# Kernel optimization log

Hardware: AMD Instinct MI355X
Metric: run time of the kernel (lower is better)

## Reference

```python
import jax, jax.numpy as jnp
import numpy as np

N, D_IN, D_OUT, NHEAD = 4096, 512, 128, 4


def setup_inputs() -> dict:
    key = jax.random.key(0)
    k1, k2, k3, k4, k5 = jax.random.split(key, 5)
    adj = jax.random.randint(k1, (N, N), 0, 2).astype(jnp.float32)  # dense binary adjacency
    x = jax.random.normal(k2, (N, D_IN), dtype=jnp.float32)
    W = jax.random.normal(k3, (D_IN, D_OUT), dtype=jnp.float32) * (1.0 / np.sqrt(D_IN))
    attn_l_w = jax.random.normal(k4, (NHEAD, D_OUT), dtype=jnp.float32) * (1.0 / np.sqrt(D_OUT))
    attn_r_w = jax.random.normal(k5, (NHEAD, D_OUT), dtype=jnp.float32) * (1.0 / np.sqrt(D_OUT))
    b = jnp.zeros((D_OUT,), dtype=jnp.float32)
    return {"adj": adj, "x": x, "W": W, "attn_l_w": attn_l_w, "attn_r_w": attn_r_w, "b": b}


def reference(adj, x, W, attn_l_w, attn_r_w, b):
    # h = x @ W : [N, D_OUT]
    h = x @ W
    el = h @ attn_l_w.T  # [N, H]  (nn.Linear(output_dim, nhead, bias=False))
    er = h @ attn_r_w.T  # [N, H]
    # Dense equivalent of nonzero-gather + index_put_ scatter into [N, N, H]:
    # attn[i, j, :] = exp(leaky_relu(el[i] + er[j])) where adj[i, j] != 0, else 0.
    e = el[:, None, :] + er[None, :, :]                      # [N, N, H]
    a = jnp.where(adj[:, :, None] != 0,
                  jnp.exp(jax.nn.leaky_relu(e, negative_slope=0.2)),
                  jnp.zeros((), dtype=e.dtype))              # [N, N, H]
    a = jnp.transpose(a, (0, 2, 1))                          # [N, H, N]
    # F.normalize(p=1, dim=-1): divide by max(L1 row sum, 1e-12); a >= 0 so L1 = sum.
    a = a / jnp.maximum(jnp.sum(a, axis=-1, keepdims=True), 1e-12)
    out = jnp.einsum('nhm,md->nhd', a, h) + b                # [N, H, D_OUT]
    return out.reshape(out.shape[0], -1)                     # flatten heads -> [N, H*D_OUT]
```

## Files before the change

kernel.cpp:

```cpp
#include <hip/hip_runtime.h>

#define NN 4096
#define DIN 512
#define DOUT 128
#define NH 4
#define LOG2E 1.44269504088896340736f

typedef __bf16 bf16x8 __attribute__((ext_vector_type(8)));
typedef float f32x4 __attribute__((ext_vector_type(4)));
typedef unsigned short u16;
typedef u16 u16x8 __attribute__((ext_vector_type(8)));
typedef u16 u16x4 __attribute__((ext_vector_type(4)));
typedef unsigned long long u64;

static __device__ __forceinline__ u16 f2bf(float f) {
  __bf16 h = (__bf16)f;
  return __builtin_bit_cast(u16, h);
}

static __device__ __forceinline__ void gl_lds16(const void* g, void* l) {
  __builtin_amdgcn_global_load_lds(
      (const __attribute__((address_space(1))) unsigned int*)g,
      (__attribute__((address_space(3))) unsigned int*)l, 16, 0, 0);
}

__global__ __launch_bounds__(256) void pack_adj(const float* __restrict__ adj,
                                                u64* __restrict__ adjW) {
  const int t = threadIdx.x;
  const int lane = t & 63;
  const int wv = t >> 6;
  const size_t blk = blockIdx.x;
  #pragma unroll
  for (int it = 0; it < 4; ++it) {
    const size_t wbase = blk * 128 + it * 32 + wv * 8;
    float v[8];
    #pragma unroll
    for (int u = 0; u < 8; ++u) v[u] = adj[(wbase + u) * 64 + lane];
    #pragma unroll
    for (int u = 0; u < 8; ++u) {
      const u64 m = __ballot(v[u] != 0.0f);
      if (lane == 0) adjW[wbase + u] = m;
    }
  }
}

__global__ __launch_bounds__(256) void prep_wt(const float* __restrict__ W,
                                               u16* __restrict__ wthi,
                                               u16* __restrict__ wtlo) {
  const int n = blockIdx.x;
  const int t = threadIdx.x;
  for (int k = t; k < 512; k += 256) {
    const float w = W[(size_t)k * 128 + n];
    const __bf16 hi = (__bf16)w;
    const float lo = w - (float)hi;
    wthi[(size_t)n * 512 + k] = __builtin_bit_cast(u16, hi);
    wtlo[(size_t)n * 512 + k] = f2bf(lo);
  }
}

__global__ __launch_bounds__(512, 1) void hcompute(
    const float* __restrict__ x, const u16* __restrict__ wthi,
    const u16* __restrict__ wtlo, const float* __restrict__ alw,
    const float* __restrict__ arw, u16* __restrict__ hT,
    float* __restrict__ el, float* __restrict__ erT) {
  __shared__ __align__(16) char pool[147456];
  const int t = threadIdx.x;
  const int i0 = blockIdx.x * 16;
  const int lane = t & 63, w = t >> 6;
  const int l15 = lane & 15, lhi = lane >> 4;

  const int xr = t >> 5, xk = (t & 31) * 4;
  const unsigned x_off =
      ((unsigned)(xr * 256 + xk * 2)) ^ ((unsigned)((xr & 7) << 4));

  f32x4 acc = (f32x4){0.f, 0.f, 0.f, 0.f};

  auto stageW = [&](int kc, int buf) {
    #pragma unroll
    for (int q = 0; q < 4; ++q) {
      const int off = q * 8192 + t * 16;
      const int n = off >> 8;
      const int kb = off & 255;
      const int ksrc = (kb ^ ((n & 7) << 4)) >> 1;
      const size_t so = (size_t)n * 512 + kc * 128 + ksrc;
      gl_lds16(wthi + so, pool + 16384 + buf * 32768 + off);
      gl_lds16(wtlo + so, pool + 81920 + buf * 32768 + off);
    }
  };
  auto writeX = [&](const float4& xv, int buf) {
    u16x4 hi, lo;
    const float* xp = (const float*)&xv;
    #pragma unroll
    for (int j = 0; j < 4; ++j) {
      const __bf16 hb = (__bf16)xp[j];
      hi[j] = __builtin_bit_cast(u16, hb);
      lo[j] = f2bf(xp[j] - (float)hb);
    }
    *(u16x4*)(pool + buf * 4096 + x_off) = hi;
    *(u16x4*)(pool + 8192 + buf * 4096 + x_off) = lo;
  };

  stageW(0, 0);
  {
    float4 xv = *(const float4*)(x + (size_t)(i0 + xr) * DIN + xk);
    writeX(xv, 0);
  }
  float4 xnext;
  for (int kc = 0; kc < 4; ++kc) {
    const int cur = kc & 1;
    __syncthreads();
    const bool more = (kc < 3);
    if (more) {
      stageW(kc + 1, cur ^ 1);
      xnext = *(const float4*)(x + (size_t)(i0 + xr) * DIN + (kc + 1) * 128 + xk);
    }
    #pragma unroll
    for (int ks = 0; ks < 4; ++ks) {
      const unsigned kbyte = (unsigned)(ks * 64 + lhi * 16);
      const unsigned xoff =
          (unsigned)(l15 * 256) + (kbyte ^ (unsigned)((l15 & 7) << 4));
      const bf16x8 ah = *(const bf16x8*)(pool + cur * 4096 + xoff);
      const bf16x8 al = *(const bf16x8*)(pool + 8192 + cur * 4096 + xoff);
      const int n = w * 16 + l15;
      const unsigned wb =
          (unsigned)(n * 256) + (kbyte ^ (unsigned)((n & 7) << 4));
      const bf16x8 bh = *(const bf16x8*)(pool + 16384 + cur * 32768 + wb);
      const bf16x8 bl = *(const bf16x8*)(pool + 81920 + cur * 32768 + wb);
      acc = __builtin_amdgcn_mfma_f32_16x16x32_bf16(ah, bh, acc, 0, 0, 0);
      acc = __builtin_amdgcn_mfma_f32_16x16x32_bf16(al, bh, acc, 0, 0, 0);
      acc = __builtin_amdgcn_mfma_f32_16x16x32_bf16(ah, bl, acc, 0, 0, 0);
    }
    if (more) writeX(xnext, cur ^ 1);
  }
  __syncthreads();
  float* h_lds = (float*)(pool + 16384);
  #pragma unroll
  for (int reg = 0; reg < 4; ++reg)
    h_lds[(lhi * 4 + reg) * 132 + w * 16 + l15] = acc[reg];
  __syncthreads();
  {
    const int d = t >> 2, ih0 = (t & 3) * 4;
    u16x4 hv;
    #pragma unroll
    for (int j = 0; j < 4; ++j) hv[j] = f2bf(h_lds[(ih0 + j) * 132 + d]);
    *(u16x4*)(hT + (size_t)d * NN + i0 + ih0) = hv;
  }
  if (t < 128) {
    const int r = t >> 3, hh = (t >> 1) & 3, side = t & 1;
    const float* wrow = (side ? arw : alw) + hh * DOUT;
    float s = 0.f;
    for (int d = 0; d < 128; ++d) s += h_lds[r * 132 + d] * wrow[d];
    s *= LOG2E;
    if (side == 0) el[(size_t)(i0 + r) * NH + hh] = s;
    else erT[(size_t)hh * NN + i0 + r] = s;
  }
}

template <int KSPLIT>
__global__ __launch_bounds__(512, 4) void gat_main(
    const unsigned char* __restrict__ adjB, const u16* __restrict__ hT,
    const float* __restrict__ el, const float* __restrict__ erT,
    const float* __restrict__ bias, float* __restrict__ outp,
    float* __restrict__ accP, float* __restrict__ SP) {
  __shared__ __align__(16) u16 A_lds[2][64 * 64];
  __shared__ __align__(16) u16 B_lds[2][128 * 64];
  __shared__ float S_lds[64];
  const int t = threadIdx.x;
  const int b = blockIdx.x;
  const int g = b & 255;
  const int ks = (KSPLIT > 1) ? (b >> 8) : 0;
  const int i0 = g * 16;
  const int jbeg = (ks * 64) / KSPLIT;
  const int jcnt = ((ks + 1) * 64) / KSPLIT - jbeg;
  const int row = t >> 3, head = row >> 4, il = row & 15;
  const float elv = el[(size_t)(i0 + il) * NH + head];
  const unsigned char* adjrow = adjB + (size_t)(i0 + il) * 512 + jbeg * 8 + (t & 7);
  const float* errow = erT + (size_t)head * NN + jbeg * 64 + (t & 7) * 8;
  const unsigned a_off =
      (unsigned)(row * 128 + (t & 7) * 16) ^ (unsigned)((row & 7) << 4);
  const int bd = t >> 3;
  const int bkb = (t & 7) * 16;
  const u16* hsrc = hT + (size_t)bd * NN + jbeg * 64 +
                    (((unsigned)bkb ^ (unsigned)((bd & 7) << 4)) >> 1);
  const int lane = t & 63, w = t >> 6;
  const int rt = w >> 1, ch = w & 1;
  const int l15 = lane & 15, lhi = lane >> 4;
  const int am = rt * 16 + l15;
  const unsigned aswz = (unsigned)((am & 7) << 4);
  f32x4 acc[4];
  #pragma unroll
  for (int ct = 0; ct < 4; ++ct) acc[ct] = (f32x4){0.f, 0.f, 0.f, 0.f};
  float Sp = 0.f;

  auto stageB = [&](int jt, int buf) {
    char* dst = (char*)B_lds[buf] + t * 16;
    gl_lds16(hsrc + jt * 64, dst);
    gl_lds16(hsrc + jt * 64 + (size_t)64 * NN, dst + 8192);
  };
  auto genA = [&](unsigned char abv, const float4& ea, const float4& eb, int buf) {
    float ev[8];
    *(float4*)ev = ea;
    *(float4*)(ev + 4) = eb;
    u16x8 pk;
    float s = 0.f;
    #pragma unroll
    for (int q = 0; q < 8; ++q) {
      const float e = elv + ev[q];
      const float l = fmaf(0.4f, __builtin_fabsf(e), 0.6f * e);
      const float ex = exp2f(l);
      const int msk = ((int)((unsigned)abv << (31 - q))) >> 31;
      const float av = __builtin_bit_cast(float, __builtin_bit_cast(int, ex) & msk);
      s += av;
      pk[q] = f2bf(av);
    }
    Sp += s;
    *(u16x8*)((char*)A_lds[buf] + a_off) = pk;
  };

  stageB(0, 0);
  {
    const unsigned char ab = adjrow[0];
    const float4 e0 = *(const float4*)errow;
    const float4 e1 = *(const float4*)(errow + 4);
    genA(ab, e0, e1, 0);
  }

  for (int jt = 0; jt < jcnt; ++jt) {
    const int cur = jt & 1;
    __syncthreads();
    const bool more = (jt + 1 < jcnt);
    unsigned char abn = 0;
    float4 e0n = {0, 0, 0, 0}, e1n = {0, 0, 0, 0};
    if (more) {
      stageB(jt + 1, cur ^ 1);
      abn = adjrow[(jt + 1) * 8];
      e0n = *(const float4*)(errow + (jt + 1) * 64);
      e1n = *(const float4*)(errow + (jt + 1) * 64 + 4);
    }
    const char* Abc = (const char*)A_lds[cur];
    const char* Bbc = (const char*)B_lds[cur];
    #pragma unroll
    for (int kk = 0; kk < 2; ++kk) {
      const unsigned kbyte = (unsigned)(kk * 64 + lhi * 16);
      const bf16x8 af = *(const bf16x8*)(Abc + (am * 128 + (kbyte ^ aswz)));
      #pragma unroll
      for (int ct = 0; ct < 4; ++ct) {
        const int col = ch * 64 + ct * 16 + l15;
        const bf16x8 bfr = *(const bf16x8*)(
            Bbc + (col * 128 + (kbyte ^ (unsigned)((col & 7) << 4))));
        acc[ct] = __builtin_amdgcn_mfma_f32_16x16x32_bf16(af, bfr, acc[ct], 0, 0, 0);
      }
    }
    if (more) genA(abn, e0n, e1n, cur ^ 1);
  }

  Sp += __shfl_xor(Sp, 1);
  Sp += __shfl_xor(Sp, 2);
  Sp += __shfl_xor(Sp, 4);

  if (KSPLIT == 1) {
    if ((t & 7) == 0) S_lds[row] = Sp;
    __syncthreads();
    #pragma unroll
    for (int reg = 0; reg < 4; ++reg) {
      const int mrow = rt * 16 + lhi * 4 + reg;
      const float inv = 1.f / fmaxf(S_lds[mrow], 1e-12f);
      const int irow = i0 + (mrow & 15);
      #pragma unroll
      for (int ct = 0; ct < 4; ++ct) {
        const int colp = ch * 64 + ct * 16 + l15;
        outp[(size_t)irow * (NH * DOUT) + rt * DOUT + colp] =
            acc[ct][reg] * inv + bias[colp];
      }
    }
  } else {
    if ((t & 7) == 0) SP[(size_t)b * 64 + row] = Sp;
    float* dst = accP + (size_t)b * 8192;
    #pragma unroll
    for (int reg = 0; reg < 4; ++reg) {
      const int mrow = rt * 16 + lhi * 4 + reg;
      #pragma unroll
      for (int ct = 0; ct < 4; ++ct) {
        const int colp = ch * 64 + ct * 16 + l15;
        dst[mrow * 128 + colp] = acc[ct][reg];
      }
    }
  }
}

template <int KS>
__global__ __launch_bounds__(256) void reduce_norm(
    const float* __restrict__ accP, const float* __restrict__ SP,
    const float* __restrict__ bias, float* __restrict__ outp) {
  const int idx = blockIdx.x * 256 + threadIdx.x;
  const int o = idx * 4;
  const int d = o & 127;
  const int hh = (o >> 7) & 3;
  const int i = o >> 9;
  const int g = i >> 4;
  const int m = hh * 16 + (i & 15);
  float4 p = make_float4(0.f, 0.f, 0.f, 0.f);
  float S = 0.f;
  #pragma unroll
  for (int s = 0; s < KS; ++s) {
    const float4 q =
        *(const float4*)(accP + (size_t)(s * 256 + g) * 8192 + m * 128 + d);
    p.x += q.x; p.y += q.y; p.z += q.z; p.w += q.w;
    S += SP[(size_t)(s * 256 + g) * 64 + m];
  }
  const float inv = 1.f / fmaxf(S, 1e-12f);
  const float4 bb = *(const float4*)(bias + d);
  float4 r;
  r.x = p.x * inv + bb.x;
  r.y = p.y * inv + bb.y;
  r.z = p.z * inv + bb.z;
  r.w = p.w * inv + bb.w;
  *(float4*)(outp + o) = r;
}

extern "C" void kernel_launch(void* const* d_in, const int* in_sizes, int n_in,
                              void* d_out, int out_size, void* d_ws, size_t ws_size,
                              hipStream_t stream) {
  const float* adj = (const float*)d_in[0];
  const float* x = (const float*)d_in[1];
  const float* W = (const float*)d_in[2];
  const float* alw = (const float*)d_in[3];
  const float* arw = (const float*)d_in[4];
  const float* bias = (const float*)d_in[5];
  float* out = (float*)d_out;
  char* ws = (char*)d_ws;
  u16* hT = (u16*)ws;
  float* el = (float*)(ws + 0x100000);
  float* erT = (float*)(ws + 0x110000);
  unsigned char* adjB = (unsigned char*)(ws + 0x120000);
  u16* wthi = (u16*)(ws + 0x320000);
  u16* wtlo = (u16*)(ws + 0x340000);
  float* accP = (float*)(ws + 0x360000);
  const size_t need3 = 0x360000ull + 768ull * 32768 + 768ull * 256;
  const size_t need2 = 0x360000ull + 512ull * 32768 + 512ull * 256;

  pack_adj<<<2048, 256, 0, stream>>>(adj, (u64*)adjB);
  prep_wt<<<128, 256, 0, stream>>>(W, wthi, wtlo);
  hcompute<<<256, 512, 0, stream>>>(x, wthi, wtlo, alw, arw, hT, el, erT);
  if (ws_size >= need3) {
    float* SP = (float*)(ws + 0x360000 + 768ull * 32768);
    gat_main<3><<<768, 512, 0, stream>>>(adjB, hT, el, erT, bias, out, accP, SP);
    reduce_norm<3><<<2048, 256, 0, stream>>>(accP, SP, bias, out);
  } else if (ws_size >= need2) {
    float* SP = (float*)(ws + 0x360000 + 512ull * 32768);
    gat_main<2><<<512, 512, 0, stream>>>(adjB, hT, el, erT, bias, out, accP, SP);
    reduce_norm<2><<<2048, 256, 0, stream>>>(accP, SP, bias, out);
  } else {
    gat_main<1><<<256, 512, 0, stream>>>(adjB, hT, el, erT, bias, out, accP, accP);
  }
}
```

Measured before the change: 170.3 us.

## Rewrite attention kernel with register-resident A, 32x32 MFMA and in-block K-split

```diff
diff --git a/kernel.cpp b/kernel.cpp
--- a/kernel.cpp
+++ b/kernel.cpp
@@ -8,10 +8,11 @@
 
 typedef __bf16 bf16x8 __attribute__((ext_vector_type(8)));
 typedef float f32x4 __attribute__((ext_vector_type(4)));
+typedef float f32x16 __attribute__((ext_vector_type(16)));
 typedef unsigned short u16;
+typedef unsigned int u32;
 typedef u16 u16x8 __attribute__((ext_vector_type(8)));
 typedef u16 u16x4 __attribute__((ext_vector_type(4)));
-typedef unsigned long long u64;
 
 static __device__ __forceinline__ u16 f2bf(float f) {
   __bf16 h = (__bf16)f;
@@ -24,37 +25,34 @@
       (__attribute__((address_space(3))) unsigned int*)l, 16, 0, 0);
 }
 
-__global__ __launch_bounds__(256) void pack_adj(const float* __restrict__ adj,
-                                                u64* __restrict__ adjW) {
+__global__ __launch_bounds__(256) void pack_prep(const float* __restrict__ adj,
+                                                 u32* __restrict__ adjW,
+                                                 const float* __restrict__ W,
+                                                 u16* __restrict__ wthi,
+                                                 u16* __restrict__ wtlo) {
+  const int b = blockIdx.x;
   const int t = threadIdx.x;
-  const int lane = t & 63;
-  const int wv = t >> 6;
-  const size_t blk = blockIdx.x;
-  #pragma unroll
-  for (int it = 0; it < 4; ++it) {
-    const size_t wbase = blk * 128 + it * 32 + wv * 8;
-    float v[8];
-    #pragma unroll
-    for (int u = 0; u < 8; ++u) v[u] = adj[(wbase + u) * 64 + lane];
-    #pragma unroll
-    for (int u = 0; u < 8; ++u) {
-      const u64 m = __ballot(v[u] != 0.0f);
-      if (lane == 0) adjW[wbase + u] = m;
-    }
-  }
-}
-
-__global__ __launch_bounds__(256) void prep_wt(const float* __restrict__ W,
-                                               u16* __restrict__ wthi,
-                                               u16* __restrict__ wtlo) {
-  const int n = blockIdx.x;
-  const int t = threadIdx.x;
-  for (int k = t; k < 512; k += 256) {
-    const float w = W[(size_t)k * 128 + n];
-    const __bf16 hi = (__bf16)w;
-    const float lo = w - (float)hi;
-    wthi[(size_t)n * 512 + k] = __builtin_bit_cast(u16, hi);
-    wtlo[(size_t)n * 512 + k] = f2bf(lo);
+  if (b < 2048) {
+    const int idx = b * 256 + t;
+    const float4* src = (const float4*)(adj + (size_t)idx * 32);
+    u32 m = 0;
+    #pragma unroll
+    for (int c = 0; c < 8; ++c) {
+      const float4 v = src[c];
+      m |= (v.x != 0.f ? 1u : 0u) << (c * 4);
+      m |= (v.y != 0.f ? 2u : 0u) << (c * 4);
+      m |= (v.z != 0.f ? 4u : 0u) << (c * 4);
+      m |= (v.w != 0.f ? 8u : 0u) << (c * 4);
+    }
+    adjW[idx] = m;
+  } else {
+    const int n = b - 2048;
+    for (int k = t; k < 512; k += 256) {
+      const float w = W[(size_t)k * 128 + n];
+      const __bf16 hi = (__bf16)w;
+      wthi[(size_t)n * 512 + k] = __builtin_bit_cast(u16, hi);
+      wtlo[(size_t)n * 512 + k] = f2bf(w - (float)hi);
+    }
   }
 }
 
@@ -156,166 +154,158 @@
   }
 }
 
-template <int KSPLIT>
-__global__ __launch_bounds__(512, 4) void gat_main(
+__global__ __launch_bounds__(512, 1) void gat_main(
     const unsigned char* __restrict__ adjB, const u16* __restrict__ hT,
     const float* __restrict__ el, const float* __restrict__ erT,
-    const float* __restrict__ bias, float* __restrict__ outp,
-    float* __restrict__ accP, float* __restrict__ SP) {
-  __shared__ __align__(16) u16 A_lds[2][64 * 64];
-  __shared__ __align__(16) u16 B_lds[2][128 * 64];
+    const float* __restrict__ bias, float* __restrict__ outp) {
+  __shared__ __align__(16) char B_lds[2][2][16384];
   __shared__ float S_lds[64];
   const int t = threadIdx.x;
-  const int b = blockIdx.x;
-  const int g = b & 255;
-  const int ks = (KSPLIT > 1) ? (b >> 8) : 0;
-  const int i0 = g * 16;
-  const int jbeg = (ks * 64) / KSPLIT;
-  const int jcnt = ((ks + 1) * 64) / KSPLIT - jbeg;
-  const int row = t >> 3, head = row >> 4, il = row & 15;
+  const int i0 = blockIdx.x * 16;
+  const int lane = t & 63;
+  const int w = t >> 6;
+  const int rt = (w >> 2) & 1;
+  const int kkg = w & 3;
+  const int l31 = lane & 31;
+  const int lh = lane >> 5;
+  const int il = l31 & 15;
+  const int head = rt * 2 + (l31 >> 4);
   const float elv = el[(size_t)(i0 + il) * NH + head];
-  const unsigned char* adjrow = adjB + (size_t)(i0 + il) * 512 + jbeg * 8 + (t & 7);
-  const float* errow = erT + (size_t)head * NN + jbeg * 64 + (t & 7) * 8;
-  const unsigned a_off =
-      (unsigned)(row * 128 + (t & 7) * 16) ^ (unsigned)((row & 7) << 4);
+  if (t < 64) S_lds[t] = 0.f;
+
   const int bd = t >> 3;
   const int bkb = (t & 7) * 16;
-  const u16* hsrc = hT + (size_t)bd * NN + jbeg * 64 +
-                    (((unsigned)bkb ^ (unsigned)((bd & 7) << 4)) >> 1);
-  const int lane = t & 63, w = t >> 6;
-  const int rt = w >> 1, ch = w & 1;
-  const int l15 = lane & 15, lhi = lane >> 4;
-  const int am = rt * 16 + l15;
-  const unsigned aswz = (unsigned)((am & 7) << 4);
-  f32x4 acc[4];
+  const u16* hsrc0 = hT + (size_t)bd * NN + (((unsigned)bkb ^ ((bd & 7) << 4)) >> 1);
+  const u16* hsrc1 = hsrc0 + (size_t)64 * NN;
+  auto stageB = [&](int tile, char* buf) {
+    gl_lds16(hsrc0 + tile * 64, buf + t * 16);
+    gl_lds16(hsrc1 + tile * 64, buf + 8192 + t * 16);
+  };
+
+  const unsigned char* adjp = adjB + (size_t)(i0 + il) * 512 + kkg * 2 + lh;
+  const float* erp = erT + (size_t)head * NN + kkg * 16 + lh * 8;
+  auto loadInputs = [&](int tile0, float4 (&e0)[2], float4 (&e1)[2], u32 (&ab)[2]) {
+    #pragma unroll
+    for (int s = 0; s < 2; ++s) {
+      e0[s] = *(const float4*)(erp + (tile0 + s) * 64);
+      e1[s] = *(const float4*)(erp + (tile0 + s) * 64 + 4);
+      ab[s] = adjp[(tile0 + s) * 8];
+    }
+  };
+
+  f32x16 acc[4];
   #pragma unroll
-  for (int ct = 0; ct < 4; ++ct) acc[ct] = (f32x4){0.f, 0.f, 0.f, 0.f};
+  for (int ct = 0; ct < 4; ++ct)
+    #pragma unroll
+    for (int q = 0; q < 16; ++q) acc[ct][q] = 0.f;
   float Sp = 0.f;
-
-  auto stageB = [&](int jt, int buf) {
-    char* dst = (char*)B_lds[buf] + t * 16;
-    gl_lds16(hsrc + jt * 64, dst);
-    gl_lds16(hsrc + jt * 64 + (size_t)64 * NN, dst + 8192);
-  };
-  auto genA = [&](unsigned char abv, const float4& ea, const float4& eb, int buf) {
-    float ev[8];
-    *(float4*)ev = ea;
-    *(float4*)(ev + 4) = eb;
-    u16x8 pk;
-    float s = 0.f;
-    #pragma unroll
-    for (int q = 0; q < 8; ++q) {
-      const float e = elv + ev[q];
-      const float l = fmaf(0.4f, __builtin_fabsf(e), 0.6f * e);
-      const float ex = exp2f(l);
-      const int msk = ((int)((unsigned)abv << (31 - q))) >> 31;
-      const float av = __builtin_bit_cast(float, __builtin_bit_cast(int, ex) & msk);
-      s += av;
-      pk[q] = f2bf(av);
-    }
-    Sp += s;
-    *(u16x8*)((char*)A_lds[buf] + a_off) = pk;
-  };
-
-  stageB(0, 0);
-  {
-    const unsigned char ab = adjrow[0];
-    const float4 e0 = *(const float4*)errow;
-    const float4 e1 = *(const float4*)(errow + 4);
-    genA(ab, e0, e1, 0);
-  }
-
-  for (int jt = 0; jt < jcnt; ++jt) {
-    const int cur = jt & 1;
+  const unsigned kb = (unsigned)(kkg * 32 + lh * 16);
+
+  float4 e0A[2], e1A[2];
+  u32 abA[2];
+  float4 e0B[2], e1B[2];
+  u32 abB[2];
+  loadInputs(0, e0A, e1A, abA);
+  stageB(0, &B_lds[0][0][0]);
+  stageB(1, &B_lds[0][1][0]);
+
+  auto phase = [&](int p, float4 (&ue0)[2], float4 (&ue1)[2], u32 (&uab)[2],
+                   float4 (&ne0)[2], float4 (&ne1)[2], u32 (&nab)[2]) {
+    const int bp = p & 1;
     __syncthreads();
-    const bool more = (jt + 1 < jcnt);
-    unsigned char abn = 0;
-    float4 e0n = {0, 0, 0, 0}, e1n = {0, 0, 0, 0};
-    if (more) {
-      stageB(jt + 1, cur ^ 1);
-      abn = adjrow[(jt + 1) * 8];
-      e0n = *(const float4*)(errow + (jt + 1) * 64);
-      e1n = *(const float4*)(errow + (jt + 1) * 64 + 4);
-    }
-    const char* Abc = (const char*)A_lds[cur];
-    const char* Bbc = (const char*)B_lds[cur];
-    #pragma unroll
-    for (int kk = 0; kk < 2; ++kk) {
-      const unsigned kbyte = (unsigned)(kk * 64 + lhi * 16);
-      const bf16x8 af = *(const bf16x8*)(Abc + (am * 128 + (kbyte ^ aswz)));
+    if (p < 31) {
+      stageB(2 * p + 2, &B_lds[bp ^ 1][0][0]);
+      stageB(2 * p + 3, &B_lds[bp ^ 1][1][0]);
+      loadInputs(2 * p + 2, ne0, ne1, nab);
+    }
+    #pragma unroll
+    for (int tl = 0; tl < 2; ++tl) {
+      float ev[8];
+      *(float4*)ev = ue0[tl];
+      *(float4*)(ev + 4) = ue1[tl];
+      u16x8 pk;
+      float s = 0.f;
+      #pragma unroll
+      for (int q = 0; q < 8; ++q) {
+        const float e = elv + ev[q];
+        const float lr = fmaxf(e, 0.2f * e);
+        const float ex = __builtin_amdgcn_exp2f(lr);
+        const int msk = ((int)(uab[tl] << (31 - q))) >> 31;
+        const float av =
+            __builtin_bit_cast(float, __builtin_bit_cast(int, ex) & msk);
+        s += av;
+        pk[q] = f2bf(av);
+      }
+      Sp += s;
+      const bf16x8 af = __builtin_bit_cast(bf16x8, pk);
+      const char* Bt = &B_lds[bp][tl][0];
+      __builtin_amdgcn_s_setprio(1);
       #pragma unroll
       for (int ct = 0; ct < 4; ++ct) {
-        const int col = ch * 64 + ct * 16 + l15;
+        const int col = ct * 32 + l31;
         const bf16x8 bfr = *(const bf16x8*)(
-            Bbc + (col * 128 + (kbyte ^ (unsigned)((col & 7) << 4))));
-        acc[ct] = __builtin_amdgcn_mfma_f32_16x16x32_bf16(af, bfr, acc[ct], 0, 0, 0);
-      }
-    }
-    if (more) genA(abn, e0n, e1n, cur ^ 1);
-  }
-
-  Sp += __shfl_xor(Sp, 1);
-  Sp += __shfl_xor(Sp, 2);
-  Sp += __shfl_xor(Sp, 4);
-
-  if (KSPLIT == 1) {
-    if ((t & 7) == 0) S_lds[row] = Sp;
-    __syncthreads();
-    #pragma unroll
-    for (int reg = 0; reg < 4; ++reg) {
-      const int mrow = rt * 16 + lhi * 4 + reg;
-      const float inv = 1.f / fmaxf(S_lds[mrow], 1e-12f);
-      const int irow = i0 + (mrow & 15);
-      #pragma unroll
-      for (int ct = 0; ct < 4; ++ct) {
-        const int colp = ch * 64 + ct * 16 + l15;
-        outp[(size_t)irow * (NH * DOUT) + rt * DOUT + colp] =
-            acc[ct][reg] * inv + bias[colp];
-      }
-    }
-  } else {
-    if ((t & 7) == 0) SP[(size_t)b * 64 + row] = Sp;
-    float* dst = accP + (size_t)b * 8192;
-    #pragma unroll
-    for (int reg = 0; reg < 4; ++reg) {
-      const int mrow = rt * 16 + lhi * 4 + reg;
-      #pragma unroll
-      for (int ct = 0; ct < 4; ++ct) {
-        const int colp = ch * 64 + ct * 16 + l15;
-        dst[mrow * 128 + colp] = acc[ct][reg];
-      }
-    }
-  }
-}
-
-template <int KS>
-__global__ __launch_bounds__(256) void reduce_norm(
-    const float* __restrict__ accP, const float* __restrict__ SP,
-    const float* __restrict__ bias, float* __restrict__ outp) {
-  const int idx = blockIdx.x * 256 + threadIdx.x;
-  const int o = idx * 4;
-  const int d = o & 127;
-  const int hh = (o >> 7) & 3;
-  const int i = o >> 9;
-  const int g = i >> 4;
-  const int m = hh * 16 + (i & 15);
-  float4 p = make_float4(0.f, 0.f, 0.f, 0.f);
-  float S = 0.f;
-  #pragma unroll
-  for (int s = 0; s < KS; ++s) {
-    const float4 q =
-        *(const float4*)(accP + (size_t)(s * 256 + g) * 8192 + m * 128 + d);
-    p.x += q.x; p.y += q.y; p.z += q.z; p.w += q.w;
-    S += SP[(size_t)(s * 256 + g) * 64 + m];
-  }
-  const float inv = 1.f / fmaxf(S, 1e-12f);
-  const float4 bb = *(const float4*)(bias + d);
-  float4 r;
-  r.x = p.x * inv + bb.x;
-  r.y = p.y * inv + bb.y;
-  r.z = p.z * inv + bb.z;
-  r.w = p.w * inv + bb.w;
-  *(float4*)(outp + o) = r;
+            Bt + col * 128 + (kb ^ ((unsigned)(col & 7) << 4)));
+        acc[ct] = __builtin_amdgcn_mfma_f32_32x32x16_bf16(af, bfr, acc[ct], 0, 0, 0);
+      }
+      __builtin_amdgcn_s_setprio(0);
+    }
+  };
+
+  for (int pp = 0; pp < 16; ++pp) {
+    phase(2 * pp, e0A, e1A, abA, e0B, e1B, abB);
+    phase(2 * pp + 1, e0B, e1B, abB, e0A, e1A, abA);
+  }
+
+  Sp += __shfl_xor(Sp, 32);
+  if (lane < 32) atomicAdd(&S_lds[rt * 32 + l31], Sp);
+
+  float* red = (float*)B_lds;
+  auto writeAcc = [&](int r) {
+    float* dst = red + r * 4096;
+    #pragma unroll
+    for (int ct = 0; ct < 4; ++ct)
+      #pragma unroll
+      for (int q4 = 0; q4 < 4; ++q4) {
+        f32x4 v;
+        #pragma unroll
+        for (int j = 0; j < 4; ++j) v[j] = acc[ct][q4 * 4 + j];
+        *(f32x4*)(dst + (ct * 4 + q4) * 256 + lane * 4) = v;
+      }
+  };
+  auto addAcc = [&](int r) {
+    const float* srcr = red + r * 4096;
+    #pragma unroll
+    for (int ct = 0; ct < 4; ++ct)
+      #pragma unroll
+      for (int q4 = 0; q4 < 4; ++q4) {
+        const f32x4 v = *(const f32x4*)(srcr + (ct * 4 + q4) * 256 + lane * 4);
+        #pragma unroll
+        for (int j = 0; j < 4; ++j) acc[ct][q4 * 4 + j] += v[j];
+      }
+  };
+  __syncthreads();
+  if (kkg >= 2) writeAcc(rt * 2 + (kkg - 2));
+  __syncthreads();
+  if (kkg < 2) addAcc(rt * 2 + kkg);
+  __syncthreads();
+  if (kkg == 1) writeAcc(rt);
+  __syncthreads();
+  if (kkg == 0) {
+    addAcc(rt);
+    #pragma unroll
+    for (int ct = 0; ct < 4; ++ct) {
+      const int col = ct * 32 + l31;
+      const float bb = bias[col];
+      #pragma unroll
+      for (int reg = 0; reg < 16; ++reg) {
+        const int crow = (reg & 3) + 8 * (reg >> 2) + 4 * lh;
+        const int mrow = rt * 32 + crow;
+        const float inv = 1.f / fmaxf(S_lds[mrow], 1e-12f);
+        outp[(size_t)(i0 + (mrow & 15)) * (NH * DOUT) + (mrow >> 4) * DOUT + col] =
+            acc[ct][reg] * inv + bb;
+      }
+    }
+  }
 }
 
 extern "C" void kernel_launch(void* const* d_in, const int* in_sizes, int n_in,
@@ -335,22 +325,8 @@
   unsigned char* adjB = (unsigned char*)(ws + 0x120000);
   u16* wthi = (u16*)(ws + 0x320000);
   u16* wtlo = (u16*)(ws + 0x340000);
-  float* accP = (float*)(ws + 0x360000);
-  const size_t need3 = 0x360000ull + 768ull * 32768 + 768ull * 256;
-  const size_t need2 = 0x360000ull + 512ull * 32768 + 512ull * 256;
-
-  pack_adj<<<2048, 256, 0, stream>>>(adj, (u64*)adjB);
-  prep_wt<<<128, 256, 0, stream>>>(W, wthi, wtlo);
+
+  pack_prep<<<2176, 256, 0, stream>>>(adj, (u32*)adjB, W, wthi, wtlo);
   hcompute<<<256, 512, 0, stream>>>(x, wthi, wtlo, alw, arw, hT, el, erT);
-  if (ws_size >= need3) {
-    float* SP = (float*)(ws + 0x360000 + 768ull * 32768);
-    gat_main<3><<<768, 512, 0, stream>>>(adjB, hT, el, erT, bias, out, accP, SP);
-    reduce_norm<3><<<2048, 256, 0, stream>>>(accP, SP, bias, out);
-  } else if (ws_size >= need2) {
-    float* SP = (float*)(ws + 0x360000 + 512ull * 32768);
-    gat_main<2><<<512, 512, 0, stream>>>(adjB, hT, el, erT, bias, out, accP, SP);
-    reduce_norm<2><<<2048, 256, 0, stream>>>(accP, SP, bias, out);
-  } else {
-    gat_main<1><<<256, 512, 0, stream>>>(adjB, hT, el, erT, bias, out, accP, accP);
-  }
-}
+  gat_main<<<256, 512, 0, stream>>>(adjB, hT, el, erT, bias, out);
+}
```

Measured after the change: 172.5 us. Within noise of the previous version (+1.3%).
